# Kernel optimization log

Hardware: AMD Instinct MI355X
Metric: run time of the kernel (lower is better)

The kernel has to match this reference:

```python
import jax, jax.numpy as jnp
import numpy as np

BN_EPS = 1e-5
NUM_GRAPHS = 64


def setup_inputs() -> dict:
    key = jax.random.key(0)
    ks = jax.random.split(key, 10)
    N, F, H, E = 50000, 128, 256, 800000
    x = jax.random.normal(ks[0], (N, F), dtype=jnp.float32)
    edge_index = jax.random.randint(ks[1], (2, E), 0, N, dtype=jnp.int64)
    batch = jnp.sort(jax.random.randint(ks[2], (N,), 0, NUM_GRAPHS, dtype=jnp.int64))
    # Linear weights stored as [in, out]; y = z @ w + b (equivalent to torch Linear)
    w1_0 = jax.random.normal(ks[3], (F, H), dtype=jnp.float32) / np.sqrt(F)
    b1_0 = jnp.zeros((H,), jnp.float32)
    w2_0 = jax.random.normal(ks[4], (H, H), dtype=jnp.float32) / np.sqrt(H)
    b2_0 = jnp.zeros((H,), jnp.float32)
    g_0 = jnp.ones((H,), jnp.float32)
    be_0 = jnp.zeros((H,), jnp.float32)
    w1_r = jax.random.normal(ks[5], (3, H, H), dtype=jnp.float32) / np.sqrt(H)
    b1_r = jnp.zeros((3, H), jnp.float32)
    w2_r = jax.random.normal(ks[6], (3, H, H), dtype=jnp.float32) / np.sqrt(H)
    b2_r = jnp.zeros((3, H), jnp.float32)
    g_r = jnp.ones((3, H), jnp.float32)
    be_r = jnp.zeros((3, H), jnp.float32)
    return dict(x=x, edge_index=edge_index, batch=batch,
                w1_0=w1_0, b1_0=b1_0, w2_0=w2_0, b2_0=b2_0, g_0=g_0, be_0=be_0,
                w1_r=w1_r, b1_r=b1_r, w2_r=w2_r, b2_r=b2_r, g_r=g_r, be_r=be_r)


def _gin_layer(h, src, dst, n, w1, b1, w2, b2, g, be):
    # GINConv with eps=0: MLP(h_i + sum_{j->i} h_j), scatter-add over edges
    agg = jax.ops.segment_sum(h[src], dst, num_segments=n)  # [N, d]
    z = agg + h
    z = jnp.maximum(z @ w1 + b1, 0.0)
    z = z @ w2 + b2
    # BatchNorm1d over the node dimension (training-mode batch statistics)
    mu = jnp.mean(z, axis=0)
    var = jnp.var(z, axis=0)
    z = (z - mu) * jax.lax.rsqrt(var + BN_EPS) * g + be
    return jnp.maximum(z, 0.0)  # ReLU; dropout is identity in eval mode


def reference(x, edge_index, batch, w1_0, b1_0, w2_0, b2_0, g_0, be_0,
              w1_r, b1_r, w2_r, b2_r, g_r, be_r):
    src, dst = edge_index[0], edge_index[1]
    n = x.shape[0]
    h = _gin_layer(x, src, dst, n, w1_0, b1_0, w2_0, b2_0, g_0, be_0)
    for i in range(3):
        h = _gin_layer(h, src, dst, n, w1_r[i], b1_r[i], w2_r[i], b2_r[i], g_r[i], be_r[i])
    # global mean pool per graph id
    counts = jax.ops.segment_sum(jnp.ones((n,), h.dtype), batch, num_segments=NUM_GRAPHS)
    pooled = jax.ops.segment_sum(h, batch, num_segments=NUM_GRAPHS)
    return pooled / jnp.maximum(counts, 1.0)[:, None]
```

## Files before the change

kernel.cpp:

```cpp
#include <hip/hip_runtime.h>

typedef float  f32x4 __attribute__((ext_vector_type(4)));
typedef _Float16 half8 __attribute__((ext_vector_type(8)));
typedef _Float16 half4 __attribute__((ext_vector_type(4)));

#define BN_EPS 1e-5f
#define NGRAPH 64

struct PrepArgs {
    const float* src[8];
    _Float16*    dst[8];
    int          K[8];
};

__global__ void prep_weights(PrepArgs a) {
    int m = blockIdx.y;
    int K = a.K[m];
    int total = K << 8;
    int idx = blockIdx.x * blockDim.x + threadIdx.x;
    if (idx >= total) return;
    int n = idx / K;
    int k = idx - n * K;
    a.dst[m][idx] = (_Float16)a.src[m][(size_t)k * 256 + n];
}

__global__ void cast_x(const float* __restrict__ x, _Float16* __restrict__ o, int total) {
    int i = (blockIdx.x * blockDim.x + threadIdx.x) << 3;
    if (i >= total) return;
    f32x4 a = *(const f32x4*)(x + i);
    f32x4 b = *(const f32x4*)(x + i + 4);
    half8 r;
#pragma unroll
    for (int k = 0; k < 4; ++k) { r[k] = (_Float16)a[k]; r[k + 4] = (_Float16)b[k]; }
    *(half8*)(o + i) = r;
}

__global__ void edge_count(const int* __restrict__ ei, int* __restrict__ cnt,
                           int* __restrict__ rank, int E) {
    int e = blockIdx.x * blockDim.x + threadIdx.x;
    if (e < E) rank[e] = atomicAdd(&cnt[ei[E + e]], 1);
}

__global__ void scan_p1(const int* __restrict__ cnt, int* __restrict__ part, int N) {
    __shared__ int lds[256];
    int idx = blockIdx.x * 256 + threadIdx.x;
    lds[threadIdx.x] = (idx < N) ? cnt[idx] : 0;
    __syncthreads();
    for (int d = 128; d > 0; d >>= 1) {
        if (threadIdx.x < d) lds[threadIdx.x] += lds[threadIdx.x + d];
        __syncthreads();
    }
    if (threadIdx.x == 0) part[blockIdx.x] = lds[0];
}

__global__ void scan_p2(int* __restrict__ part, int* __restrict__ off, int N, int nb) {
    __shared__ int lds[256];
    int t = threadIdx.x;
    int v = (t < nb) ? part[t] : 0;
    lds[t] = v;
    __syncthreads();
    for (int d = 1; d < 256; d <<= 1) {
        int a = (t >= d) ? lds[t - d] : 0;
        __syncthreads();
        lds[t] += a;
        __syncthreads();
    }
    if (t < nb) part[t] = lds[t] - v;
    if (t == nb - 1) off[N] = lds[t];
}

__global__ void scan_p3(const int* __restrict__ cnt, const int* __restrict__ part,
                        int* __restrict__ off, int N) {
    __shared__ int lds[256];
    int t = threadIdx.x;
    int idx = blockIdx.x * 256 + t;
    int v = (idx < N) ? cnt[idx] : 0;
    lds[t] = v;
    __syncthreads();
    for (int d = 1; d < 256; d <<= 1) {
        int a = (t >= d) ? lds[t - d] : 0;
        __syncthreads();
        lds[t] += a;
        __syncthreads();
    }
    if (idx < N) off[idx] = part[blockIdx.x] + lds[t] - v;
}

__global__ void edge_fill(const int* __restrict__ ei, const int* __restrict__ off,
                          const int* __restrict__ rank, int* __restrict__ csr_src, int E) {
    int e = blockIdx.x * blockDim.x + threadIdx.x;
    if (e >= E) return;
    csr_src[off[ei[E + e]] + rank[e]] = ei[e];
}

__global__ void gather0(const _Float16* __restrict__ x, const int* __restrict__ off,
                        const int* __restrict__ srcs, _Float16* __restrict__ out, int N) {
    int wid = (blockIdx.x << 2) + (threadIdx.x >> 6);
    if (wid >= N) return;
    int lane = threadIdx.x & 63;
    int q = lane >> 4;
    int fb = (lane & 15) << 3;
    float acc[8] = {0.f, 0.f, 0.f, 0.f, 0.f, 0.f, 0.f, 0.f};
    int end = off[wid + 1];
    int e = off[wid] + q;
    for (; e + 4 < end; e += 8) {
        int s0 = srcs[e], s1 = srcs[e + 4];
        half8 v0 = *(const half8*)(x + (size_t)s0 * 128 + fb);
        half8 v1 = *(const half8*)(x + (size_t)s1 * 128 + fb);
#pragma unroll
        for (int k = 0; k < 8; ++k) acc[k] += (float)v0[k] + (float)v1[k];
    }
    if (e < end) {
        int s0 = srcs[e];
        half8 v0 = *(const half8*)(x + (size_t)s0 * 128 + fb);
#pragma unroll
        for (int k = 0; k < 8; ++k) acc[k] += (float)v0[k];
    }
    if (q == 0) {
        half8 v = *(const half8*)(x + (size_t)wid * 128 + fb);
#pragma unroll
        for (int k = 0; k < 8; ++k) acc[k] += (float)v[k];
    }
#pragma unroll
    for (int k = 0; k < 8; ++k) {
        acc[k] += __shfl_xor(acc[k], 16);
        acc[k] += __shfl_xor(acc[k], 32);
    }
    if (q == 0) {
        half8 o;
#pragma unroll
        for (int k = 0; k < 8; ++k) o[k] = (_Float16)acc[k];
        *(half8*)(out + (size_t)wid * 128 + fb) = o;
    }
}

__global__ void gather_fused(const _Float16* __restrict__ z, const int* __restrict__ off,
                             const int* __restrict__ srcs, const float* __restrict__ stats,
                             const float* __restrict__ gam, const float* __restrict__ bet,
                             _Float16* __restrict__ out, int N, float invN) {
    int wid = (blockIdx.x << 2) + (threadIdx.x >> 6);
    if (wid >= N) return;
    int lane = threadIdx.x & 63;
    int hf = lane >> 5;
    int fb = (lane & 31) << 3;
    half8 sc8, tc8;
#pragma unroll
    for (int k = 0; k < 8; ++k) {
        float mu = stats[fb + k] * invN;
        float var = stats[256 + fb + k] * invN - mu * mu;
        float s = gam[fb + k] * rsqrtf(var + BN_EPS);
        sc8[k] = (_Float16)s;
        tc8[k] = (_Float16)(bet[fb + k] - mu * s);
    }
    const half8 zero8 = {0, 0, 0, 0, 0, 0, 0, 0};
    float acc[8] = {0.f, 0.f, 0.f, 0.f, 0.f, 0.f, 0.f, 0.f};
    int end = off[wid + 1];
    int e = off[wid] + hf;
    for (; e + 6 < end; e += 8) {
        int s0 = srcs[e], s1 = srcs[e + 2], s2 = srcs[e + 4], s3 = srcs[e + 6];
        half8 v0 = *(const half8*)(z + (size_t)s0 * 256 + fb);
        half8 v1 = *(const half8*)(z + (size_t)s1 * 256 + fb);
        half8 v2 = *(const half8*)(z + (size_t)s2 * 256 + fb);
        half8 v3 = *(const half8*)(z + (size_t)s3 * 256 + fb);
        half8 r0 = __builtin_elementwise_max(v0 * sc8 + tc8, zero8);
        half8 r1 = __builtin_elementwise_max(v1 * sc8 + tc8, zero8);
        half8 r2 = __builtin_elementwise_max(v2 * sc8 + tc8, zero8);
        half8 r3 = __builtin_elementwise_max(v3 * sc8 + tc8, zero8);
#pragma unroll
        for (int k = 0; k < 8; ++k)
            acc[k] += ((float)r0[k] + (float)r1[k]) + ((float)r2[k] + (float)r3[k]);
    }
    for (; e < end; e += 2) {
        int s0 = srcs[e];
        half8 v0 = *(const half8*)(z + (size_t)s0 * 256 + fb);
        half8 r0 = __builtin_elementwise_max(v0 * sc8 + tc8, zero8);
#pragma unroll
        for (int k = 0; k < 8; ++k) acc[k] += (float)r0[k];
    }
    if (hf == 0) {
        half8 v = *(const half8*)(z + (size_t)wid * 256 + fb);
        half8 r = __builtin_elementwise_max(v * sc8 + tc8, zero8);
#pragma unroll
        for (int k = 0; k < 8; ++k) acc[k] += (float)r[k];
    }
#pragma unroll
    for (int k = 0; k < 8; ++k) acc[k] += __shfl_xor(acc[k], 32);
    if (hf == 0) {
        half8 o;
#pragma unroll
        for (int k = 0; k < 8; ++k) o[k] = (_Float16)acc[k];
        *(half8*)(out + (size_t)wid * 256 + fb) = o;
    }
}

template <int K, int WITH_STATS>
__global__ __launch_bounds__(512, 2) void gemm_kernel(
    const _Float16* __restrict__ A, const _Float16* __restrict__ BT,
    const float* __restrict__ bias, _Float16* __restrict__ Y,
    float* __restrict__ stats, int M) {
    extern __shared__ _Float16 blds[];
    const int tid = threadIdx.x;
    const int colbase = blockIdx.y * 128;
    {
        int row = tid >> 2, q = tid & 3, kq = q * (K / 4);
        const _Float16* src = BT + (size_t)(colbase + row) * K + kq;
        _Float16* dst = blds + row * K;
        int sw = (row & 7) << 3;
#pragma unroll
        for (int c = 0; c < K / 4; c += 8)
            *(half8*)(dst + ((kq + c) ^ sw)) = *(const half8*)(src + c);
    }
    __syncthreads();

    const int lane = tid & 63, wave = tid >> 6;
    const int i = lane & 15, g = lane >> 4;
    const int rowbase = blockIdx.x * 128 + wave * 16;
    const int arow = min(rowbase + i, M - 1);

    half8 afrag[K / 32];
#pragma unroll
    for (int s = 0; s < K / 32; ++s)
        afrag[s] = *(const half8*)(A + (size_t)arow * K + s * 32 + g * 8);

    f32x4 acc[8];
#pragma unroll
    for (int t = 0; t < 8; ++t) acc[t] = (f32x4){0.f, 0.f, 0.f, 0.f};

    const int sw = (i & 7) << 3;
#pragma unroll
    for (int s = 0; s < K / 32; ++s)
#pragma unroll
        for (int t = 0; t < 8; ++t) {
            half8 b = *(const half8*)(blds + (t * 16 + i) * K + ((s * 32 + g * 8) ^ sw));
            acc[t] = __builtin_amdgcn_mfma_f32_16x16x32_f16(afrag[s], b, acc[t], 0, 0, 0);
        }
    __syncthreads();

    _Float16* ostage = blds;
    float* sred = (float*)(blds + 17408);
    const int rg = g * 4;
#pragma unroll
    for (int t = 0; t < 8; ++t) {
        int c = t * 16 + i;
        float bv = bias[colbase + c];
        float s1 = 0.f, s2 = 0.f;
#pragma unroll
        for (int j = 0; j < 4; ++j) {
            float v = acc[t][j] + bv;
            if (WITH_STATS == 0) v = fmaxf(v, 0.f);
            ostage[(wave * 16 + rg + j) * 136 + c] = (_Float16)v;
            if (WITH_STATS) {
                if (rowbase + rg + j < M) { s1 += v; s2 += v * v; }
            }
        }
        if (WITH_STATS) {
            s1 += __shfl_xor(s1, 16); s1 += __shfl_xor(s1, 32);
            s2 += __shfl_xor(s2, 16); s2 += __shfl_xor(s2, 32);
            if (g == 0) {
                sred[wave * 128 + c] = s1;
                sred[1024 + wave * 128 + c] = s2;
            }
        }
    }
    __syncthreads();
    if (WITH_STATS && tid < 256) {
        int which = tid >> 7, c = tid & 127;
        float s = 0.f;
#pragma unroll
        for (int w = 0; w < 8; ++w) s += sred[which * 1024 + w * 128 + c];
        atomicAdd(&stats[which * 256 + colbase + c], s);
    }
#pragma unroll
    for (int k = 0; k < 4; ++k) {
        int ch = k * 512 + tid;
        int rl = ch >> 4, pc = (ch & 15) << 3;
        int r = blockIdx.x * 128 + rl;
        if (r < M)
            *(half8*)(Y + (size_t)r * 256 + colbase + pc) =
                *(const half8*)(ostage + rl * 136 + pc);
    }
}

__global__ void graph_bounds(const int* __restrict__ batch, int* __restrict__ gstart, int N) {
    int t = threadIdx.x;
    if (t > NGRAPH) return;
    if (t == NGRAPH) { gstart[t] = N; return; }
    int lo = 0, hi = N;
    while (lo < hi) { int m = (lo + hi) >> 1; if (batch[m] < t) lo = m + 1; else hi = m; }
    gstart[t] = lo;
}

#define PCHUNK 256
__global__ void pool_stage1(const _Float16* __restrict__ z, const int* __restrict__ batch,
                            const int* __restrict__ gstart, const float* __restrict__ stats,
                            const float* __restrict__ gam, const float* __restrict__ bet,
                            float* __restrict__ acc, int N, float invN) {
    __shared__ float lds[8 * 512];
    int c0 = blockIdx.x * PCHUNK;
    int cend = min(c0 + PCHUNK, N);
    int tid = threadIdx.x;
    int rowlane = tid >> 5;
    int fb = (tid & 31) << 3;
    float sc[8], tc[8];
#pragma unroll
    for (int k = 0; k < 8; ++k) {
        float mu = stats[fb + k] * invN;
        float var = stats[256 + fb + k] * invN - mu * mu;
        float s = gam[fb + k] * rsqrtf(var + BN_EPS);
        sc[k] = s;
        tc[k] = bet[fb + k] - mu * s;
    }
    int segs = c0;
    while (segs < cend) {
        int g = batch[segs];
        int sege = min(gstart[g + 1], cend);
        float a[8] = {0.f, 0.f, 0.f, 0.f, 0.f, 0.f, 0.f, 0.f};
        for (int r = segs + rowlane; r < sege; r += 16) {
            half8 v = *(const half8*)(z + (size_t)r * 256 + fb);
#pragma unroll
            for (int k = 0; k < 8; ++k)
                a[k] += fmaxf(fmaf((float)v[k], sc[k], tc[k]), 0.f);
        }
#pragma unroll
        for (int k = 0; k < 8; ++k) lds[k * 512 + tid] = a[k];
        __syncthreads();
#pragma unroll
        for (int d = 8; d > 0; d >>= 1) {
            if (rowlane < d) {
#pragma unroll
                for (int k = 0; k < 8; ++k)
                    lds[k * 512 + tid] += lds[k * 512 + tid + d * 32];
            }
            __syncthreads();
        }
        if (rowlane == 0) {
#pragma unroll
            for (int k = 0; k < 8; ++k)
                atomicAdd(&acc[g * 256 + fb + k], lds[k * 512 + tid]);
        }
        __syncthreads();
        segs = sege;
    }
}

__global__ void pool_finalize(const float* __restrict__ acc, const int* __restrict__ gstart,
                              float* __restrict__ out) {
    int i = blockIdx.x * 256 + threadIdx.x;
    int g = i >> 8;
    int c = gstart[g + 1] - gstart[g];
    out[i] = acc[i] / (float)(c > 0 ? c : 1);
}

extern "C" void kernel_launch(void* const* d_in, const int* in_sizes, int n_in,
                              void* d_out, int out_size, void* d_ws, size_t ws_size,
                              hipStream_t stream) {
    const float* x    = (const float*)d_in[0];
    const int*   ei   = (const int*)d_in[1];
    const int*   batch= (const int*)d_in[2];
    const float* w1_0 = (const float*)d_in[3];
    const float* b1_0 = (const float*)d_in[4];
    const float* w2_0 = (const float*)d_in[5];
    const float* b2_0 = (const float*)d_in[6];
    const float* g_0  = (const float*)d_in[7];
    const float* be_0 = (const float*)d_in[8];
    const float* w1_r = (const float*)d_in[9];
    const float* b1_r = (const float*)d_in[10];
    const float* w2_r = (const float*)d_in[11];
    const float* b2_r = (const float*)d_in[12];
    const float* g_r  = (const float*)d_in[13];
    const float* be_r = (const float*)d_in[14];

    const int N = in_sizes[0] / 128;
    const int E = in_sizes[1] / 2;

    char* p = (char*)d_ws;
    auto alloc = [&](size_t bytes) { char* r = p; p += (bytes + 255) & ~(size_t)255; return r; };
    float*    stats   = (float*)alloc(4 * 512 * sizeof(float));
    int*      part    = (int*)alloc(256 * sizeof(int));
    int*      off     = (int*)alloc((size_t)(N + 1) * sizeof(int));
    int*      cnt     = (int*)alloc((size_t)N * sizeof(int));
    int*      gstart  = (int*)alloc(65 * sizeof(int));
    float*    accp    = (float*)alloc(NGRAPH * 256 * sizeof(float));
    int*      rank    = (int*)alloc((size_t)E * sizeof(int));
    int*      csr_src = (int*)alloc((size_t)E * sizeof(int));
    _Float16* wT      = (_Float16*)alloc((size_t)491520 * sizeof(_Float16));
    _Float16* x16     = (_Float16*)alloc((size_t)N * 128 * sizeof(_Float16));
    _Float16* zin     = (_Float16*)alloc((size_t)N * 256 * sizeof(_Float16));
    _Float16* y       = (_Float16*)alloc((size_t)N * 256 * sizeof(_Float16));
    _Float16* z       = (_Float16*)alloc((size_t)N * 256 * sizeof(_Float16));

    hipMemsetAsync(stats, 0, 4 * 512 * sizeof(float), stream);
    hipMemsetAsync(cnt, 0, (size_t)N * sizeof(int), stream);
    hipMemsetAsync(accp, 0, NGRAPH * 256 * sizeof(float), stream);

    PrepArgs pa;
    pa.src[0] = w1_0;  pa.dst[0] = wT;           pa.K[0] = 128;
    pa.src[1] = w2_0;  pa.dst[1] = wT + 32768;   pa.K[1] = 256;
    for (int i = 0; i < 3; ++i) {
        pa.src[2 + i] = w1_r + (size_t)i * 65536; pa.dst[2 + i] = wT + 98304 + (size_t)i * 65536; pa.K[2 + i] = 256;
        pa.src[5 + i] = w2_r + (size_t)i * 65536; pa.dst[5 + i] = wT + 294912 + (size_t)i * 65536; pa.K[5 + i] = 256;
    }
    prep_weights<<<dim3(256, 8), 256, 0, stream>>>(pa);
    cast_x<<<(N * 128 / 8 + 255) / 256, 256, 0, stream>>>(x, x16, N * 128);

    const int eb = (E + 255) / 256;
    const int nb = (N + 255) / 256;
    edge_count<<<eb, 256, 0, stream>>>(ei, cnt, rank, E);
    scan_p1<<<nb, 256, 0, stream>>>(cnt, part, N);
    scan_p2<<<1, 256, 0, stream>>>(part, off, N, nb);
    scan_p3<<<nb, 256, 0, stream>>>(cnt, part, off, N);
    edge_fill<<<eb, 256, 0, stream>>>(ei, off, rank, csr_src, E);
    graph_bounds<<<1, 128, 0, stream>>>(batch, gstart, N);

    const int gwb = (N + 3) / 4;
    const dim3 gemmg((N + 127) / 128, 2);
    const int lds128 = 43008;
    const int lds256 = 65536;
    const float invN = 1.0f / (float)N;

    gather0<<<gwb, 256, 0, stream>>>(x16, off, csr_src, zin, N);
    gemm_kernel<128, 0><<<gemmg, 512, lds128, stream>>>(zin, wT, b1_0, y, nullptr, N);
    gemm_kernel<256, 1><<<gemmg, 512, lds256, stream>>>(y, wT + 32768, b2_0, z, stats, N);

    const float* cur_stats = stats;
    const float* cur_g = g_0;
    const float* cur_be = be_0;
    for (int i = 0; i < 3; ++i) {
        gather_fused<<<gwb, 256, 0, stream>>>(z, off, csr_src, cur_stats, cur_g, cur_be, zin, N, invN);
        gemm_kernel<256, 0><<<gemmg, 512, lds256, stream>>>(
            zin, wT + 98304 + (size_t)i * 65536, b1_r + i * 256, y, nullptr, N);
        gemm_kernel<256, 1><<<gemmg, 512, lds256, stream>>>(
            y, wT + 294912 + (size_t)i * 65536, b2_r + i * 256, z, stats + (i + 1) * 512, N);
        cur_stats = stats + (i + 1) * 512;
        cur_g = g_r + i * 256;
        cur_be = be_r + i * 256;
    }

    pool_stage1<<<(N + PCHUNK - 1) / PCHUNK, 512, 0, stream>>>(
        z, batch, gstart, cur_stats, cur_g, cur_be, accp, N, invN);
    pool_finalize<<<NGRAPH, 256, 0, stream>>>(accp, gstart, (float*)d_out);
}
```

Baseline: 525.4 us.

## Compute full 256-column GEMM tiles per block with K-chunked weight staging

The GEMM now has each block compute all 256 output columns, so every A row is loaded once instead of twice. The weight matrix is streamed into LDS in 64-wide K chunks, which shrinks the LDS footprint, and launch bounds are raised to allow more resident blocks. The output is written in two staged halves. Separately, both gather kernels unroll deeper (4 or 8 neighbours per iteration) and use 32-bit byte-offset addressing, to put more loads in flight and cut 64-bit address arithmetic. Holding 16 accumulator tiles per wave raises register pressure, which may conflict with the higher occupancy target, and the extra chunk barriers add synchronisation.

Result: faster. 476.0 us (-9.4%).

```diff
diff --git a/kernel.cpp b/kernel.cpp
--- a/kernel.cpp
+++ b/kernel.cpp
@@ -2,7 +2,6 @@
 
 typedef float  f32x4 __attribute__((ext_vector_type(4)));
 typedef _Float16 half8 __attribute__((ext_vector_type(8)));
-typedef _Float16 half4 __attribute__((ext_vector_type(4)));
 
 #define BN_EPS 1e-5f
 #define NGRAPH 64
@@ -100,24 +99,33 @@
     int lane = threadIdx.x & 63;
     int q = lane >> 4;
     int fb = (lane & 15) << 3;
+    const char* xb = (const char*)x;
     float acc[8] = {0.f, 0.f, 0.f, 0.f, 0.f, 0.f, 0.f, 0.f};
     int end = off[wid + 1];
     int e = off[wid] + q;
+    unsigned fb2 = (unsigned)fb << 1;
+    for (; e + 12 < end; e += 16) {
+        half8 v0 = *(const half8*)(xb + (((unsigned)srcs[e] << 8) + fb2));
+        half8 v1 = *(const half8*)(xb + (((unsigned)srcs[e + 4] << 8) + fb2));
+        half8 v2 = *(const half8*)(xb + (((unsigned)srcs[e + 8] << 8) + fb2));
+        half8 v3 = *(const half8*)(xb + (((unsigned)srcs[e + 12] << 8) + fb2));
+#pragma unroll
+        for (int k = 0; k < 8; ++k)
+            acc[k] += ((float)v0[k] + (float)v1[k]) + ((float)v2[k] + (float)v3[k]);
+    }
     for (; e + 4 < end; e += 8) {
-        int s0 = srcs[e], s1 = srcs[e + 4];
-        half8 v0 = *(const half8*)(x + (size_t)s0 * 128 + fb);
-        half8 v1 = *(const half8*)(x + (size_t)s1 * 128 + fb);
+        half8 v0 = *(const half8*)(xb + (((unsigned)srcs[e] << 8) + fb2));
+        half8 v1 = *(const half8*)(xb + (((unsigned)srcs[e + 4] << 8) + fb2));
 #pragma unroll
         for (int k = 0; k < 8; ++k) acc[k] += (float)v0[k] + (float)v1[k];
     }
     if (e < end) {
-        int s0 = srcs[e];
-        half8 v0 = *(const half8*)(x + (size_t)s0 * 128 + fb);
+        half8 v0 = *(const half8*)(xb + (((unsigned)srcs[e] << 8) + fb2));
 #pragma unroll
         for (int k = 0; k < 8; ++k) acc[k] += (float)v0[k];
     }
     if (q == 0) {
-        half8 v = *(const half8*)(x + (size_t)wid * 128 + fb);
+        half8 v = *(const half8*)(xb + (((unsigned)wid << 8) + fb2));
 #pragma unroll
         for (int k = 0; k < 8; ++k) acc[k] += (float)v[k];
     }
@@ -153,32 +161,54 @@
         tc8[k] = (_Float16)(bet[fb + k] - mu * s);
     }
     const half8 zero8 = {0, 0, 0, 0, 0, 0, 0, 0};
+    const char* zb = (const char*)z;
+    unsigned fb2 = (unsigned)fb << 1;
     float acc[8] = {0.f, 0.f, 0.f, 0.f, 0.f, 0.f, 0.f, 0.f};
     int end = off[wid + 1];
     int e = off[wid] + hf;
-    for (; e + 6 < end; e += 8) {
-        int s0 = srcs[e], s1 = srcs[e + 2], s2 = srcs[e + 4], s3 = srcs[e + 6];
-        half8 v0 = *(const half8*)(z + (size_t)s0 * 256 + fb);
-        half8 v1 = *(const half8*)(z + (size_t)s1 * 256 + fb);
-        half8 v2 = *(const half8*)(z + (size_t)s2 * 256 + fb);
-        half8 v3 = *(const half8*)(z + (size_t)s3 * 256 + fb);
+    for (; e + 14 < end; e += 16) {
+        half8 v0 = *(const half8*)(zb + (((unsigned)srcs[e] << 9) + fb2));
+        half8 v1 = *(const half8*)(zb + (((unsigned)srcs[e + 2] << 9) + fb2));
+        half8 v2 = *(const half8*)(zb + (((unsigned)srcs[e + 4] << 9) + fb2));
+        half8 v3 = *(const half8*)(zb + (((unsigned)srcs[e + 6] << 9) + fb2));
+        half8 v4 = *(const half8*)(zb + (((unsigned)srcs[e + 8] << 9) + fb2));
+        half8 v5 = *(const half8*)(zb + (((unsigned)srcs[e + 10] << 9) + fb2));
+        half8 v6 = *(const half8*)(zb + (((unsigned)srcs[e + 12] << 9) + fb2));
+        half8 v7 = *(const half8*)(zb + (((unsigned)srcs[e + 14] << 9) + fb2));
         half8 r0 = __builtin_elementwise_max(v0 * sc8 + tc8, zero8);
         half8 r1 = __builtin_elementwise_max(v1 * sc8 + tc8, zero8);
         half8 r2 = __builtin_elementwise_max(v2 * sc8 + tc8, zero8);
         half8 r3 = __builtin_elementwise_max(v3 * sc8 + tc8, zero8);
+        half8 r4 = __builtin_elementwise_max(v4 * sc8 + tc8, zero8);
+        half8 r5 = __builtin_elementwise_max(v5 * sc8 + tc8, zero8);
+        half8 r6 = __builtin_elementwise_max(v6 * sc8 + tc8, zero8);
+        half8 r7 = __builtin_elementwise_max(v7 * sc8 + tc8, zero8);
+#pragma unroll
+        for (int k = 0; k < 8; ++k)
+            acc[k] += (((float)r0[k] + (float)r1[k]) + ((float)r2[k] + (float)r3[k]))
+                    + (((float)r4[k] + (float)r5[k]) + ((float)r6[k] + (float)r7[k]));
+    }
+    for (; e + 6 < end; e += 8) {
+        half8 v0 = *(const half8*)(zb + (((unsigned)srcs[e] << 9) + fb2));
+        half8 v1 = *(const half8*)(zb + (((unsigned)srcs[e + 2] << 9) + fb2));
+        half8 v2 = *(const half8*)(zb + (((unsigned)srcs[e + 4] << 9) + fb2));
+        half8 v3 = *(const half8*)(zb + (((unsigned)srcs[e + 6] << 9) + fb2));
+        half8 r0 = __builtin_elementwise_max(v0 * sc8 + tc8, zero8);
+        half8 r1 = __builtin_elementwise_max(v1 * sc8 + tc8, zero8);
+        half8 r2 = __builtin_elementwise_max(v2 * sc8 + tc8, zero8);
+        half8 r3 = __builtin_elementwise_max(v3 * sc8 + tc8, zero8);
 #pragma unroll
         for (int k = 0; k < 8; ++k)
             acc[k] += ((float)r0[k] + (float)r1[k]) + ((float)r2[k] + (float)r3[k]);
     }
     for (; e < end; e += 2) {
-        int s0 = srcs[e];
-        half8 v0 = *(const half8*)(z + (size_t)s0 * 256 + fb);
+        half8 v0 = *(const half8*)(zb + (((unsigned)srcs[e] << 9) + fb2));
         half8 r0 = __builtin_elementwise_max(v0 * sc8 + tc8, zero8);
 #pragma unroll
         for (int k = 0; k < 8; ++k) acc[k] += (float)r0[k];
     }
     if (hf == 0) {
-        half8 v = *(const half8*)(z + (size_t)wid * 256 + fb);
+        half8 v = *(const half8*)(zb + (((unsigned)wid << 9) + fb2));
         half8 r = __builtin_elementwise_max(v * sc8 + tc8, zero8);
 #pragma unroll
         for (int k = 0; k < 8; ++k) acc[k] += (float)r[k];
@@ -194,24 +224,13 @@
 }
 
 template <int K, int WITH_STATS>
-__global__ __launch_bounds__(512, 2) void gemm_kernel(
+__global__ __launch_bounds__(512, 4) void gemm_kernel(
     const _Float16* __restrict__ A, const _Float16* __restrict__ BT,
     const float* __restrict__ bias, _Float16* __restrict__ Y,
     float* __restrict__ stats, int M) {
     extern __shared__ _Float16 blds[];
+    float* sred = (float*)(blds + 17408);
     const int tid = threadIdx.x;
-    const int colbase = blockIdx.y * 128;
-    {
-        int row = tid >> 2, q = tid & 3, kq = q * (K / 4);
-        const _Float16* src = BT + (size_t)(colbase + row) * K + kq;
-        _Float16* dst = blds + row * K;
-        int sw = (row & 7) << 3;
-#pragma unroll
-        for (int c = 0; c < K / 4; c += 8)
-            *(half8*)(dst + ((kq + c) ^ sw)) = *(const half8*)(src + c);
-    }
-    __syncthreads();
-
     const int lane = tid & 63, wave = tid >> 6;
     const int i = lane & 15, g = lane >> 4;
     const int rowbase = blockIdx.x * 128 + wave * 16;
@@ -222,62 +241,93 @@
     for (int s = 0; s < K / 32; ++s)
         afrag[s] = *(const half8*)(A + (size_t)arow * K + s * 32 + g * 8);
 
-    f32x4 acc[8];
-#pragma unroll
-    for (int t = 0; t < 8; ++t) acc[t] = (f32x4){0.f, 0.f, 0.f, 0.f};
-
-    const int sw = (i & 7) << 3;
-#pragma unroll
-    for (int s = 0; s < K / 32; ++s)
-#pragma unroll
-        for (int t = 0; t < 8; ++t) {
-            half8 b = *(const half8*)(blds + (t * 16 + i) * K + ((s * 32 + g * 8) ^ sw));
-            acc[t] = __builtin_amdgcn_mfma_f32_16x16x32_f16(afrag[s], b, acc[t], 0, 0, 0);
-        }
-    __syncthreads();
-
-    _Float16* ostage = blds;
-    float* sred = (float*)(blds + 17408);
+    f32x4 acc[16];
+#pragma unroll
+    for (int t = 0; t < 16; ++t) acc[t] = (f32x4){0.f, 0.f, 0.f, 0.f};
+
+    const int scol = tid >> 1;
+    const int shalf = (tid & 1) * 32;
+    const int ssw = (scol & 7) << 3;
+    const int swi = (i & 7) << 3;
+
+#pragma unroll
+    for (int kc = 0; kc < K / 64; ++kc) {
+        if (kc) __syncthreads();
+        {
+            const _Float16* src = BT + (size_t)scol * K + kc * 64 + shalf;
+            _Float16* dst = blds + scol * 64;
+#pragma unroll
+            for (int c = 0; c < 32; c += 8)
+                *(half8*)(dst + ((shalf + c) ^ ssw)) = *(const half8*)(src + c);
+        }
+        __syncthreads();
+#pragma unroll
+        for (int ks = 0; ks < 2; ++ks)
+#pragma unroll
+            for (int t = 0; t < 16; ++t) {
+                half8 b = *(const half8*)(blds + (t * 16 + i) * 64 + ((ks * 32 + g * 8) ^ swi));
+                acc[t] = __builtin_amdgcn_mfma_f32_16x16x32_f16(afrag[kc * 2 + ks], b, acc[t], 0, 0, 0);
+            }
+    }
+
     const int rg = g * 4;
-#pragma unroll
-    for (int t = 0; t < 8; ++t) {
-        int c = t * 16 + i;
-        float bv = bias[colbase + c];
-        float s1 = 0.f, s2 = 0.f;
-#pragma unroll
-        for (int j = 0; j < 4; ++j) {
-            float v = acc[t][j] + bv;
-            if (WITH_STATS == 0) v = fmaxf(v, 0.f);
-            ostage[(wave * 16 + rg + j) * 136 + c] = (_Float16)v;
-            if (WITH_STATS) {
-                if (rowbase + rg + j < M) { s1 += v; s2 += v * v; }
+    if (WITH_STATS) {
+#pragma unroll
+        for (int t = 0; t < 16; ++t) {
+            int c = t * 16 + i;
+            float bv = bias[c];
+            float s1 = 0.f, s2 = 0.f;
+#pragma unroll
+            for (int j = 0; j < 4; ++j) {
+                if (rowbase + rg + j < M) {
+                    float v = acc[t][j] + bv;
+                    s1 += v;
+                    s2 += v * v;
+                }
             }
-        }
-        if (WITH_STATS) {
             s1 += __shfl_xor(s1, 16); s1 += __shfl_xor(s1, 32);
             s2 += __shfl_xor(s2, 16); s2 += __shfl_xor(s2, 32);
             if (g == 0) {
-                sred[wave * 128 + c] = s1;
-                sred[1024 + wave * 128 + c] = s2;
+                sred[wave * 256 + c] = s1;
+                sred[2048 + wave * 256 + c] = s2;
             }
         }
     }
     __syncthreads();
-    if (WITH_STATS && tid < 256) {
-        int which = tid >> 7, c = tid & 127;
+    if (WITH_STATS) {
+        int which = tid >> 8, c = tid & 255;
         float s = 0.f;
 #pragma unroll
-        for (int w = 0; w < 8; ++w) s += sred[which * 1024 + w * 128 + c];
-        atomicAdd(&stats[which * 256 + colbase + c], s);
-    }
-#pragma unroll
-    for (int k = 0; k < 4; ++k) {
-        int ch = k * 512 + tid;
-        int rl = ch >> 4, pc = (ch & 15) << 3;
-        int r = blockIdx.x * 128 + rl;
-        if (r < M)
-            *(half8*)(Y + (size_t)r * 256 + colbase + pc) =
-                *(const half8*)(ostage + rl * 136 + pc);
+        for (int w = 0; w < 8; ++w) s += sred[which * 2048 + w * 256 + c];
+        atomicAdd(&stats[which * 256 + c], s);
+    }
+
+    _Float16* ostage = blds;
+#pragma unroll
+    for (int ph = 0; ph < 2; ++ph) {
+        if (ph) __syncthreads();
+#pragma unroll
+        for (int tt = 0; tt < 8; ++tt) {
+            int t = ph * 8 + tt;
+            int lc = tt * 16 + i;
+            float bv = bias[t * 16 + i];
+#pragma unroll
+            for (int j = 0; j < 4; ++j) {
+                float v = acc[t][j] + bv;
+                if (WITH_STATS == 0) v = fmaxf(v, 0.f);
+                ostage[(wave * 16 + rg + j) * 136 + lc] = (_Float16)v;
+            }
+        }
+        __syncthreads();
+#pragma unroll
+        for (int k = 0; k < 4; ++k) {
+            int ch = k * 512 + tid;
+            int rl = ch >> 4, pc = (ch & 15) << 3;
+            int r = blockIdx.x * 128 + rl;
+            if (r < M)
+                *(half8*)(Y + (size_t)r * 256 + ph * 128 + pc) =
+                    *(const half8*)(ostage + rl * 136 + pc);
+        }
     }
 }
 
@@ -413,23 +463,22 @@
     graph_bounds<<<1, 128, 0, stream>>>(batch, gstart, N);
 
     const int gwb = (N + 3) / 4;
-    const dim3 gemmg((N + 127) / 128, 2);
-    const int lds128 = 43008;
-    const int lds256 = 65536;
+    const int gemmg = (N + 127) / 128;
+    const int ldsb = 51200;
     const float invN = 1.0f / (float)N;
 
     gather0<<<gwb, 256, 0, stream>>>(x16, off, csr_src, zin, N);
-    gemm_kernel<128, 0><<<gemmg, 512, lds128, stream>>>(zin, wT, b1_0, y, nullptr, N);
-    gemm_kernel<256, 1><<<gemmg, 512, lds256, stream>>>(y, wT + 32768, b2_0, z, stats, N);
+    gemm_kernel<128, 0><<<gemmg, 512, ldsb, stream>>>(zin, wT, b1_0, y, nullptr, N);
+    gemm_kernel<256, 1><<<gemmg, 512, ldsb, stream>>>(y, wT + 32768, b2_0, z, stats, N);
 
     const float* cur_stats = stats;
     const float* cur_g = g_0;
     const float* cur_be = be_0;
     for (int i = 0; i < 3; ++i) {
         gather_fused<<<gwb, 256, 0, stream>>>(z, off, csr_src, cur_stats, cur_g, cur_be, zin, N, invN);
-        gemm_kernel<256, 0><<<gemmg, 512, lds256, stream>>>(
+        gemm_kernel<256, 0><<<gemmg, 512, ldsb, stream>>>(
             zin, wT + 98304 + (size_t)i * 65536, b1_r + i * 256, y, nullptr, N);
-        gemm_kernel<256, 1><<<gemmg, 512, lds256, stream>>>(
+        gemm_kernel<256, 1><<<gemmg, 512, ldsb, stream>>>(
             y, wT + 294912 + (size_t)i * 65536, b2_r + i * 256, z, stats + (i + 1) * 512, N);
         cur_stats = stats + (i + 1) * 512;
         cur_g = g_r + i * 256;
```
